# Optimization experiments

Measured on AMD Instinct MI355X. Metric: run time of the kernel, lower is better.

Reference implementation:

```python
import jax, jax.numpy as jnp
import numpy as np

TARGET_RADIUS = 0.99
EPS = 1e-8


def _spectral_norm_wh(W_h):
    # 3-step power iteration (detached, as in torch no_grad), then scale W_h
    # so its spectral radius is ~TARGET_RADIUS. sigma keeps grad through W_h.
    D = W_h.shape[0]
    u = jax.random.normal(jax.random.key(42), (D,), dtype=W_h.dtype)
    u = u / jnp.linalg.norm(u)
    Wd = jax.lax.stop_gradient(W_h)
    v = u
    for _ in range(3):
        v = Wd.T @ u
        v = v / (jnp.linalg.norm(v) + EPS)
        u = Wd @ v
        u = u / (jnp.linalg.norm(u) + EPS)
    sigma = jnp.abs(u @ W_h @ v)
    return W_h * (TARGET_RADIUS / (sigma + EPS))


def setup_inputs() -> dict:
    key = jax.random.key(0)
    T, B, D = 256, 64, 2048
    ks = jax.random.split(key, 5)
    std = 0.02  # ~xavier scale for D=2048 is sqrt(2/(2D))~0.022
    return {
        "x": jax.random.normal(ks[0], (T, B, D), dtype=jnp.float32),
        "z": jax.random.normal(ks[1], (T, B, D), dtype=jnp.float32),
        "h0": jnp.zeros((B, D), dtype=jnp.float32),
        "W_x": jax.random.normal(ks[2], (D, D), dtype=jnp.float32) * std,
        "W_h": jax.random.normal(ks[3], (D, D), dtype=jnp.float32) * std,
        "W_gate": jax.random.normal(ks[4], (D, D), dtype=jnp.float32) * std,
        "b": jnp.zeros((D,), dtype=jnp.float32),
    }


def reference(x, z, h0, W_x, W_h, W_gate, b):
    # h_t = tanh(W_x@x_t + (W_h@h_{t-1}) * sigmoid(W_gate@x_t) + b)
    # out_t = h_t * silu(z_t)
    W_h_eff = _spectral_norm_wh(W_h)
    # Precompute input projections as one big GEMM over T*B (same math).
    xWx = jnp.einsum("tbd,ed->tbe", x, W_x) + b          # [T,B,D]
    gate = jax.nn.sigmoid(jnp.einsum("tbd,ed->tbe", x, W_gate))  # [T,B,D]
    silu_z = jax.nn.silu(z)                               # [T,B,D]

    def step(h_prev, inp):
        xw_t, g_t, sz_t = inp
        Rh = h_prev @ W_h_eff.T                           # [B,D]
        h_new = jnp.tanh(xw_t + Rh * g_t)
        out_t = h_new * sz_t
        return h_new, (h_new, out_t)

    _, (hs, output) = jax.lax.scan(step, h0, (xWx, gate, silu_z))
    h = jnp.concatenate([h0[None], hs], axis=0)           # [T+1,B,D]
    return output, h
```

## Files before the change

### kernel.cpp

```cpp
#include <hip/hip_runtime.h>
#include <hip/hip_cooperative_groups.h>
#include <cstdint>
#include <cmath>

namespace cg = cooperative_groups;


static constexpr int Tt = 256;
static constexpr int Bb = 64;
static constexpr int Dk = 2048;
static constexpr int Mrows = Tt * Bb;
static constexpr float EPSF = 1e-8f;
static constexpr float TARGET_RADIUS = 0.99f;

__device__ __forceinline__ void tf_round(uint32_t& x0, uint32_t& x1, int r) {
    x0 += x1;
    x1 = (x1 << r) | (x1 >> (32 - r));
    x1 ^= x0;
}

__device__ __forceinline__ uint2 threefry2x32(uint32_t ks0, uint32_t ks1,
                                              uint32_t x0, uint32_t x1) {
    uint32_t ks2 = ks0 ^ ks1 ^ 0x1BD11BDAu;
    x0 += ks0; x1 += ks1;
    tf_round(x0,x1,13); tf_round(x0,x1,15); tf_round(x0,x1,26); tf_round(x0,x1,6);
    x0 += ks1; x1 += ks2 + 1u;
    tf_round(x0,x1,17); tf_round(x0,x1,29); tf_round(x0,x1,16); tf_round(x0,x1,24);
    x0 += ks2; x1 += ks0 + 2u;
    tf_round(x0,x1,13); tf_round(x0,x1,15); tf_round(x0,x1,26); tf_round(x0,x1,6);
    x0 += ks0; x1 += ks1 + 3u;
    tf_round(x0,x1,17); tf_round(x0,x1,29); tf_round(x0,x1,16); tf_round(x0,x1,24);
    x0 += ks1; x1 += ks2 + 4u;
    tf_round(x0,x1,13); tf_round(x0,x1,15); tf_round(x0,x1,26); tf_round(x0,x1,6);
    x0 += ks2; x1 += ks0 + 5u;
    return make_uint2(x0, x1);
}

__global__ __launch_bounds__(256) void k_rng(float* __restrict__ u) {
    __shared__ float red[256];
    __shared__ float s_inv;
    float local = 0.f;
    for (int i = threadIdx.x; i < Dk; i += 256) {
        uint2 r = threefry2x32(0u, 42u, 0u, (uint32_t)i);
        uint32_t bits = r.x ^ r.y;
        uint32_t fb = (bits >> 9) | 0x3f800000u;
        float f01 = __uint_as_float(fb) - 1.0f;
        const float lo = -0.99999994f;
        float uu = f01 * (1.0f - lo) + lo;
        uu = fmaxf(lo, uu);
        float g = 1.41421356237f * erfinvf(uu);
        u[i] = g;
        local += g * g;
    }
    red[threadIdx.x] = local;
    __syncthreads();
    for (int s = 128; s > 0; s >>= 1) {
        if (threadIdx.x < s) red[threadIdx.x] += red[threadIdx.x + s];
        __syncthreads();
    }
    if (threadIdx.x == 0) s_inv = 1.0f / sqrtf(red[0]);
    __syncthreads();
    float inv = s_inv;
    for (int i = threadIdx.x; i < Dk; i += 256) u[i] *= inv;
}

__global__ __launch_bounds__(256) void k_matvec_T(const float* __restrict__ W,
                                                  const float* __restrict__ u,
                                                  float* __restrict__ out) {
    __shared__ float us[Dk];
    for (int i = threadIdx.x; i < Dk; i += 256) us[i] = u[i];
    __syncthreads();
    int j = blockIdx.x * 256 + threadIdx.x;
    float acc = 0.f;
    for (int i = 0; i < Dk; ++i) acc += W[(size_t)i * Dk + j] * us[i];
    out[j] = acc;
}

__global__ __launch_bounds__(256) void k_matvec_N(const float* __restrict__ W,
                                                  const float* __restrict__ v,
                                                  float* __restrict__ out) {
    __shared__ float red[256];
    const float* Wr = W + (size_t)blockIdx.x * Dk;
    float acc = 0.f;
    for (int j = threadIdx.x; j < Dk; j += 256) acc += Wr[j] * v[j];
    red[threadIdx.x] = acc;
    __syncthreads();
    for (int s = 128; s > 0; s >>= 1) {
        if (threadIdx.x < s) red[threadIdx.x] += red[threadIdx.x + s];
        __syncthreads();
    }
    if (threadIdx.x == 0) out[blockIdx.x] = red[0];
}

__global__ __launch_bounds__(256) void k_normalize(float* __restrict__ vec) {
    __shared__ float red[256];
    __shared__ float s_inv;
    float acc = 0.f;
    for (int i = threadIdx.x; i < Dk; i += 256) { float x = vec[i]; acc += x * x; }
    red[threadIdx.x] = acc;
    __syncthreads();
    for (int s = 128; s > 0; s >>= 1) {
        if (threadIdx.x < s) red[threadIdx.x] += red[threadIdx.x + s];
        __syncthreads();
    }
    if (threadIdx.x == 0) s_inv = 1.0f / (sqrtf(red[0]) + EPSF);
    __syncthreads();
    float inv = s_inv;
    for (int i = threadIdx.x; i < Dk; i += 256) vec[i] *= inv;
}

__global__ __launch_bounds__(256) void k_sigma(const float* __restrict__ uraw,
                                               float* __restrict__ scale_out) {
    __shared__ float red[256];
    float acc = 0.f;
    for (int i = threadIdx.x; i < Dk; i += 256) { float x = uraw[i]; acc += x * x; }
    red[threadIdx.x] = acc;
    __syncthreads();
    for (int s = 128; s > 0; s >>= 1) {
        if (threadIdx.x < s) red[threadIdx.x] += red[threadIdx.x + s];
        __syncthreads();
    }
    if (threadIdx.x == 0) {
        float ss = red[0];
        float n = sqrtf(ss);
        float sigma = ss / (n + EPSF);
        scale_out[0] = TARGET_RADIUS / (sigma + EPSF);
    }
}

__global__ __launch_bounds__(256, 2) void k_dualgemm(const float* __restrict__ X,
                                                     const float* __restrict__ Wx,
                                                     const float* __restrict__ Wg,
                                                     const float* __restrict__ bias,
                                                     float* __restrict__ xw_out,
                                                     float* __restrict__ gate_out) {
    __shared__ float As [16][132];
    __shared__ float Bxs[16][132];
    __shared__ float Bgs[16][132];

    const int tid = threadIdx.x;
    const int bm = blockIdx.x;
    const int bn = blockIdx.y;
    const int tx = tid & 15;
    const int ty = tid >> 4;

    float accX[8][8] = {};
    float accG[8][8] = {};

    const int lrow = tid >> 2;
    const int lk4  = (tid & 3) << 2;
    const float* Xp0  = X  + (size_t)(bm * 128 + lrow) * Dk + lk4;
    const float* Xp1  = Xp0 + (size_t)64 * Dk;
    const float* Wxp0 = Wx + (size_t)(bn * 128 + lrow) * Dk + lk4;
    const float* Wxp1 = Wxp0 + (size_t)64 * Dk;
    const float* Wgp0 = Wg + (size_t)(bn * 128 + lrow) * Dk + lk4;
    const float* Wgp1 = Wgp0 + (size_t)64 * Dk;

    for (int k0 = 0; k0 < Dk; k0 += 16) {
        float4 xa0 = *(const float4*)(Xp0  + k0);
        float4 xa1 = *(const float4*)(Xp1  + k0);
        float4 wx0 = *(const float4*)(Wxp0 + k0);
        float4 wx1 = *(const float4*)(Wxp1 + k0);
        float4 wg0 = *(const float4*)(Wgp0 + k0);
        float4 wg1 = *(const float4*)(Wgp1 + k0);
        __syncthreads();
        As [lk4 + 0][lrow]      = xa0.x; As [lk4 + 1][lrow]      = xa0.y;
        As [lk4 + 2][lrow]      = xa0.z; As [lk4 + 3][lrow]      = xa0.w;
        As [lk4 + 0][lrow + 64] = xa1.x; As [lk4 + 1][lrow + 64] = xa1.y;
        As [lk4 + 2][lrow + 64] = xa1.z; As [lk4 + 3][lrow + 64] = xa1.w;
        Bxs[lk4 + 0][lrow]      = wx0.x; Bxs[lk4 + 1][lrow]      = wx0.y;
        Bxs[lk4 + 2][lrow]      = wx0.z; Bxs[lk4 + 3][lrow]      = wx0.w;
        Bxs[lk4 + 0][lrow + 64] = wx1.x; Bxs[lk4 + 1][lrow + 64] = wx1.y;
        Bxs[lk4 + 2][lrow + 64] = wx1.z; Bxs[lk4 + 3][lrow + 64] = wx1.w;
        Bgs[lk4 + 0][lrow]      = wg0.x; Bgs[lk4 + 1][lrow]      = wg0.y;
        Bgs[lk4 + 2][lrow]      = wg0.z; Bgs[lk4 + 3][lrow]      = wg0.w;
        Bgs[lk4 + 0][lrow + 64] = wg1.x; Bgs[lk4 + 1][lrow + 64] = wg1.y;
        Bgs[lk4 + 2][lrow + 64] = wg1.z; Bgs[lk4 + 3][lrow + 64] = wg1.w;
        __syncthreads();
#pragma unroll
        for (int kk = 0; kk < 16; ++kk) {
            const float4 a0 = *(const float4*)&As [kk][ty * 8];
            const float4 a1 = *(const float4*)&As [kk][ty * 8 + 4];
            const float4 x0 = *(const float4*)&Bxs[kk][tx * 8];
            const float4 x1 = *(const float4*)&Bxs[kk][tx * 8 + 4];
            const float4 g0 = *(const float4*)&Bgs[kk][tx * 8];
            const float4 g1 = *(const float4*)&Bgs[kk][tx * 8 + 4];
            float av[8] = {a0.x, a0.y, a0.z, a0.w, a1.x, a1.y, a1.z, a1.w};
            float xv[8] = {x0.x, x0.y, x0.z, x0.w, x1.x, x1.y, x1.z, x1.w};
            float gv[8] = {g0.x, g0.y, g0.z, g0.w, g1.x, g1.y, g1.z, g1.w};
#pragma unroll
            for (int i = 0; i < 8; ++i)
#pragma unroll
                for (int j = 0; j < 8; ++j) {
                    accX[i][j] = fmaf(av[i], xv[j], accX[i][j]);
                    accG[i][j] = fmaf(av[i], gv[j], accG[i][j]);
                }
        }
    }

    const int m0 = bm * 128 + ty * 8;
    const int n0 = bn * 128 + tx * 8;
    float4 bv0 = *(const float4*)(bias + n0);
    float4 bv1 = *(const float4*)(bias + n0 + 4);
#pragma unroll
    for (int i = 0; i < 8; ++i) {
        float4 xo0, xo1, go0, go1;
        xo0.x = accX[i][0] + bv0.x; xo0.y = accX[i][1] + bv0.y;
        xo0.z = accX[i][2] + bv0.z; xo0.w = accX[i][3] + bv0.w;
        xo1.x = accX[i][4] + bv1.x; xo1.y = accX[i][5] + bv1.y;
        xo1.z = accX[i][6] + bv1.z; xo1.w = accX[i][7] + bv1.w;
        go0.x = 1.0f / (1.0f + expf(-accG[i][0]));
        go0.y = 1.0f / (1.0f + expf(-accG[i][1]));
        go0.z = 1.0f / (1.0f + expf(-accG[i][2]));
        go0.w = 1.0f / (1.0f + expf(-accG[i][3]));
        go1.x = 1.0f / (1.0f + expf(-accG[i][4]));
        go1.y = 1.0f / (1.0f + expf(-accG[i][5]));
        go1.z = 1.0f / (1.0f + expf(-accG[i][6]));
        go1.w = 1.0f / (1.0f + expf(-accG[i][7]));
        float* xrow = xw_out   + (size_t)(m0 + i) * Dk + n0;
        float* grow = gate_out + (size_t)(m0 + i) * Dk + n0;
        *(float4*)xrow       = xo0;
        *(float4*)(xrow + 4) = xo1;
        *(float4*)grow       = go0;
        *(float4*)(grow + 4) = go1;
    }
}

__global__ __launch_bounds__(256) void k_recur(const float* __restrict__ Wh,
                                               const float* __restrict__ scale_p,
                                               const float* __restrict__ z,
                                               float* __restrict__ out,
                                               float* __restrict__ hbuf) {
    cg::grid_group grid = cg::this_grid();
    __shared__ float Ws[8][2564];

    const int tid = threadIdx.x;
    const int e0 = blockIdx.x * 8;
    const float sc = scale_p[0];

    for (int idx = tid; idx < 8 * 512; idx += 256) {
        const int r = idx >> 9;
        const int c = (idx & 511) << 2;
        float4 w = *(const float4*)(Wh + (size_t)(e0 + r) * Dk + c);
        Ws[r][c + 0] = w.x * sc; Ws[r][c + 1] = w.y * sc;
        Ws[r][c + 2] = w.z * sc; Ws[r][c + 3] = w.w * sc;
    }
    __syncthreads();

    const int e = tid & 7;
    const int brow = tid >> 3;
    const float* wr = &Ws[e][0];
    const size_t BD = (size_t)Bb * Dk;
    const size_t i0 = (size_t)brow * Dk + e0 + e;
    const size_t i1 = i0 + (size_t)32 * Dk;

    for (int t = 0; t < Tt; ++t) {
        const float* hbase = hbuf + (size_t)t * BD;
        float* hg = hbuf + (size_t)(t + 1) * BD;
        float* xo = out  + (size_t)t * BD;
        const float* zt = z + (size_t)t * BD;

        float g0 = hg[i0], g1 = hg[i1];
        float x0 = xo[i0], x1 = xo[i1];
        float z0 = zt[i0], z1 = zt[i1];

        const float* hp0 = hbase + (size_t)brow * Dk;
        const float* hp1 = hp0 + (size_t)32 * Dk;
        float s00 = 0.f, s01 = 0.f, s10 = 0.f, s11 = 0.f;
#pragma unroll 4
        for (int d = 0; d < Dk; d += 8) {
            float4 w0 = *(const float4*)(wr + d);
            float4 w1 = *(const float4*)(wr + d + 4);
            float4 a0 = *(const float4*)(hp0 + d);
            float4 a1 = *(const float4*)(hp0 + d + 4);
            float4 b0 = *(const float4*)(hp1 + d);
            float4 b1 = *(const float4*)(hp1 + d + 4);
            s00 = fmaf(a0.w, w0.w, fmaf(a0.z, w0.z, fmaf(a0.y, w0.y, fmaf(a0.x, w0.x, s00))));
            s01 = fmaf(a1.w, w1.w, fmaf(a1.z, w1.z, fmaf(a1.y, w1.y, fmaf(a1.x, w1.x, s01))));
            s10 = fmaf(b0.w, w0.w, fmaf(b0.z, w0.z, fmaf(b0.y, w0.y, fmaf(b0.x, w0.x, s10))));
            s11 = fmaf(b1.w, w1.w, fmaf(b1.z, w1.z, fmaf(b1.y, w1.y, fmaf(b1.x, w1.x, s11))));
        }
        float r0 = s00 + s01;
        float r1 = s10 + s11;

        float hn0 = tanhf(x0 + r0 * g0);
        float hn1 = tanhf(x1 + r1 * g1);
        float sz0 = z0 / (1.0f + expf(-z0));
        float sz1 = z1 / (1.0f + expf(-z1));
        hg[i0] = hn0; xo[i0] = hn0 * sz0;
        hg[i1] = hn1; xo[i1] = hn1 * sz1;

        if (t + 1 < Tt) grid.sync();
    }
}

extern "C" void kernel_launch(void* const* d_in, const int* in_sizes, int n_in,
                              void* d_out, int out_size, void* d_ws, size_t ws_size,
                              hipStream_t stream) {
    const float* x    = (const float*)d_in[0];
    const float* z    = (const float*)d_in[1];
    const float* h0   = (const float*)d_in[2];
    const float* Wx   = (const float*)d_in[3];
    const float* Wh   = (const float*)d_in[4];
    const float* Wg   = (const float*)d_in[5];
    const float* bias = (const float*)d_in[6];

    float* out  = (float*)d_out;
    float* hbuf = out + (size_t)Tt * Bb * Dk;

    float* ws    = (float*)d_ws;
    float* u     = ws;
    float* v     = ws + 2048;
    float* tmp   = ws + 4096;
    float* scale = ws + 6144;

    const size_t BD = (size_t)Bb * Dk;

    hipMemcpyAsync(hbuf, h0, BD * sizeof(float), hipMemcpyDeviceToDevice, stream);

    k_rng<<<1, 256, 0, stream>>>(u);
    float* uc = u;
    float* ut = tmp;
    for (int it = 0; it < 3; ++it) {
        k_matvec_T<<<8, 256, 0, stream>>>(Wh, uc, v);
        k_normalize<<<1, 256, 0, stream>>>(v);
        k_matvec_N<<<2048, 256, 0, stream>>>(Wh, v, ut);
        if (it < 2) {
            k_normalize<<<1, 256, 0, stream>>>(ut);
            float* t2 = uc; uc = ut; ut = t2;
        }
    }
    k_sigma<<<1, 256, 0, stream>>>(ut, scale);

    dim3 gg(Mrows / 128, Dk / 128);
    k_dualgemm<<<gg, 256, 0, stream>>>(x, Wx, Wg, bias, out, hbuf + BD);

    {
        const float* aWh = Wh;
        const float* aSc = scale;
        const float* aZ  = z;
        float* aOut = out;
        float* aH   = hbuf;
        void* kargs[] = {(void*)&aWh, (void*)&aSc, (void*)&aZ,
                         (void*)&aOut, (void*)&aH};
        hipLaunchCooperativeKernel(k_recur, dim3(256), dim3(256), kargs, 0, stream);
    }
}
```

Before: 20.04 ms.

## Hold W_h slice in registers and split K across threads in recurrence

The cooperative recurrence kernel now runs 512 threads per block. Each thread keeps a 32-wide K-slice of its W_h row in registers, replacing the shared-memory copy of the whole row. Each thread computes partial dot products against all 64 batch rows, and these are reduced with an xor-shuffle butterfly followed by a small shared-memory sum across waves. The aim is to spread the per-step matvec over more threads and remove the long serial 2048-length loop per thread, at the cost of more h loads per thread and extra reduction work. A per-timestep fallback kernel is added in case the cooperative launch fails.

```diff
diff --git a/kernel.cpp b/kernel.cpp
--- a/kernel.cpp
+++ b/kernel.cpp
@@ -226,69 +226,186 @@
     }
 }
 
-__global__ __launch_bounds__(256) void k_recur(const float* __restrict__ Wh,
-                                               const float* __restrict__ scale_p,
-                                               const float* __restrict__ z,
-                                               float* __restrict__ out,
-                                               float* __restrict__ hbuf) {
+__global__ __launch_bounds__(256) void k_step(const float* __restrict__ Wh,
+                                              const float* __restrict__ scale_p,
+                                              const float* __restrict__ z_t,
+                                              float* __restrict__ xw_t,
+                                              const float* __restrict__ h_prev,
+                                              float* __restrict__ hg_t) {
+    __shared__ float Hs[32][36];
+    __shared__ float Ws[32][36];
+    const int tid = threadIdx.x;
+    const int bn = blockIdx.x;
+    const int bb = blockIdx.y;
+    const int tx = tid & 15;
+    const int ty = tid >> 4;
+
+    float a00 = 0.f, a01 = 0.f, a10 = 0.f, a11 = 0.f;
+
+    const int lrow = tid >> 3;
+    const int lk4  = (tid & 7) * 4;
+    const float* Hp = h_prev + (size_t)(bb * 32 + lrow) * Dk + lk4;
+    const float* Wp = Wh     + (size_t)(bn * 32 + lrow) * Dk + lk4;
+
+    for (int k0 = 0; k0 < Dk; k0 += 32) {
+        float4 ha = *(const float4*)(Hp + k0);
+        float4 wa = *(const float4*)(Wp + k0);
+        __syncthreads();
+        Hs[lk4 + 0][lrow] = ha.x; Hs[lk4 + 1][lrow] = ha.y;
+        Hs[lk4 + 2][lrow] = ha.z; Hs[lk4 + 3][lrow] = ha.w;
+        Ws[lk4 + 0][lrow] = wa.x; Ws[lk4 + 1][lrow] = wa.y;
+        Ws[lk4 + 2][lrow] = wa.z; Ws[lk4 + 3][lrow] = wa.w;
+        __syncthreads();
+#pragma unroll
+        for (int kk = 0; kk < 32; ++kk) {
+            float2 hv = *(const float2*)&Hs[kk][ty * 2];
+            float2 wv = *(const float2*)&Ws[kk][tx * 2];
+            a00 += hv.x * wv.x; a01 += hv.x * wv.y;
+            a10 += hv.y * wv.x; a11 += hv.y * wv.y;
+        }
+    }
+
+    const float sc = scale_p[0];
+    const int e0 = bn * 32 + tx * 2;
+    const int b0 = bb * 32 + ty * 2;
+    float acc[2][2] = {{a00, a01}, {a10, a11}};
+#pragma unroll
+    for (int i = 0; i < 2; ++i)
+#pragma unroll
+        for (int j = 0; j < 2; ++j) {
+            size_t idx = (size_t)(b0 + i) * Dk + (e0 + j);
+            float Rh = acc[i][j] * sc;
+            float g = hg_t[idx];
+            float pre = xw_t[idx] + Rh * g;
+            float hn = tanhf(pre);
+            float zv = z_t[idx];
+            float sz = zv / (1.0f + expf(-zv));
+            hg_t[idx] = hn;
+            xw_t[idx] = hn * sz;
+        }
+}
+
+__global__ __launch_bounds__(512, 2) void k_recur(const float* __restrict__ Wh,
+                                                  const float* __restrict__ scale_p,
+                                                  const float* __restrict__ z,
+                                                  float* __restrict__ out,
+                                                  float* __restrict__ hbuf) {
     cg::grid_group grid = cg::this_grid();
-    __shared__ float Ws[8][2564];
+    __shared__ float red[8 * 576];
 
     const int tid = threadIdx.x;
     const int e0 = blockIdx.x * 8;
+    const int c  = tid & 7;
+    const int ks = tid >> 3;
+    const int k0 = ks * 32;
+    const int wv = tid >> 6;
     const float sc = scale_p[0];
 
-    for (int idx = tid; idx < 8 * 512; idx += 256) {
-        const int r = idx >> 9;
-        const int c = (idx & 511) << 2;
-        float4 w = *(const float4*)(Wh + (size_t)(e0 + r) * Dk + c);
-        Ws[r][c + 0] = w.x * sc; Ws[r][c + 1] = w.y * sc;
-        Ws[r][c + 2] = w.z * sc; Ws[r][c + 3] = w.w * sc;
-    }
-    __syncthreads();
-
-    const int e = tid & 7;
-    const int brow = tid >> 3;
-    const float* wr = &Ws[e][0];
+    float w[32];
+    {
+        const float* wp = Wh + (size_t)(e0 + c) * Dk + k0;
+#pragma unroll
+        for (int j = 0; j < 8; ++j) {
+            float4 v = *(const float4*)(wp + 4 * j);
+            w[4*j+0] = v.x * sc; w[4*j+1] = v.y * sc;
+            w[4*j+2] = v.z * sc; w[4*j+3] = v.w * sc;
+        }
+    }
+
+    const int rr = ((tid >> 3) & 1) * 8 + ((tid >> 4) & 1) * 4 + ((tid >> 5) & 1) * 2;
+    const int wbase = wv * 576 + rr * 9 + c;
+
+    const int r_out = tid >> 3;
     const size_t BD = (size_t)Bb * Dk;
-    const size_t i0 = (size_t)brow * Dk + e0 + e;
-    const size_t i1 = i0 + (size_t)32 * Dk;
+    const size_t oidx = (size_t)r_out * Dk + e0 + c;
+    const int rbase = r_out * 9 + c;
+
+    const bool hi3 = (tid & 8)  != 0;
+    const bool hi4 = (tid & 16) != 0;
+    const bool hi5 = (tid & 32) != 0;
 
     for (int t = 0; t < Tt; ++t) {
-        const float* hbase = hbuf + (size_t)t * BD;
+        const float* hb = hbuf + (size_t)t * BD;
         float* hg = hbuf + (size_t)(t + 1) * BD;
         float* xo = out  + (size_t)t * BD;
         const float* zt = z + (size_t)t * BD;
 
-        float g0 = hg[i0], g1 = hg[i1];
-        float x0 = xo[i0], x1 = xo[i1];
-        float z0 = zt[i0], z1 = zt[i1];
-
-        const float* hp0 = hbase + (size_t)brow * Dk;
-        const float* hp1 = hp0 + (size_t)32 * Dk;
-        float s00 = 0.f, s01 = 0.f, s10 = 0.f, s11 = 0.f;
-#pragma unroll 4
-        for (int d = 0; d < Dk; d += 8) {
-            float4 w0 = *(const float4*)(wr + d);
-            float4 w1 = *(const float4*)(wr + d + 4);
-            float4 a0 = *(const float4*)(hp0 + d);
-            float4 a1 = *(const float4*)(hp0 + d + 4);
-            float4 b0 = *(const float4*)(hp1 + d);
-            float4 b1 = *(const float4*)(hp1 + d + 4);
-            s00 = fmaf(a0.w, w0.w, fmaf(a0.z, w0.z, fmaf(a0.y, w0.y, fmaf(a0.x, w0.x, s00))));
-            s01 = fmaf(a1.w, w1.w, fmaf(a1.z, w1.z, fmaf(a1.y, w1.y, fmaf(a1.x, w1.x, s01))));
-            s10 = fmaf(b0.w, w0.w, fmaf(b0.z, w0.z, fmaf(b0.y, w0.y, fmaf(b0.x, w0.x, s10))));
-            s11 = fmaf(b1.w, w1.w, fmaf(b1.z, w1.z, fmaf(b1.y, w1.y, fmaf(b1.x, w1.x, s11))));
-        }
-        float r0 = s00 + s01;
-        float r1 = s10 + s11;
-
-        float hn0 = tanhf(x0 + r0 * g0);
-        float hn1 = tanhf(x1 + r1 * g1);
-        float sz0 = z0 / (1.0f + expf(-z0));
-        float sz1 = z1 / (1.0f + expf(-z1));
-        hg[i0] = hn0; xo[i0] = hn0 * sz0;
-        hg[i1] = hn1; xo[i1] = hn1 * sz1;
+        float gv = hg[oidx];
+        float xv = xo[oidx];
+        float zv = zt[oidx];
+
+#pragma unroll 1
+        for (int g = 0; g < 4; ++g) {
+            float acc[16];
+            const float* hp = hb + (size_t)(g * 16) * Dk + k0;
+#pragma unroll
+            for (int r = 0; r < 16; ++r) {
+                const float* hr = hp + (size_t)r * Dk;
+                float4 h0 = *(const float4*)(hr + 0);
+                float4 h1 = *(const float4*)(hr + 4);
+                float4 h2 = *(const float4*)(hr + 8);
+                float4 h3 = *(const float4*)(hr + 12);
+                float4 h4 = *(const float4*)(hr + 16);
+                float4 h5 = *(const float4*)(hr + 20);
+                float4 h6 = *(const float4*)(hr + 24);
+                float4 h7 = *(const float4*)(hr + 28);
+                float s0 = 0.f, s1 = 0.f;
+                s0 = fmaf(h0.x, w[0], s0);  s1 = fmaf(h0.y, w[1], s1);
+                s0 = fmaf(h0.z, w[2], s0);  s1 = fmaf(h0.w, w[3], s1);
+                s0 = fmaf(h1.x, w[4], s0);  s1 = fmaf(h1.y, w[5], s1);
+                s0 = fmaf(h1.z, w[6], s0);  s1 = fmaf(h1.w, w[7], s1);
+                s0 = fmaf(h2.x, w[8], s0);  s1 = fmaf(h2.y, w[9], s1);
+                s0 = fmaf(h2.z, w[10], s0); s1 = fmaf(h2.w, w[11], s1);
+                s0 = fmaf(h3.x, w[12], s0); s1 = fmaf(h3.y, w[13], s1);
+                s0 = fmaf(h3.z, w[14], s0); s1 = fmaf(h3.w, w[15], s1);
+                s0 = fmaf(h4.x, w[16], s0); s1 = fmaf(h4.y, w[17], s1);
+                s0 = fmaf(h4.z, w[18], s0); s1 = fmaf(h4.w, w[19], s1);
+                s0 = fmaf(h5.x, w[20], s0); s1 = fmaf(h5.y, w[21], s1);
+                s0 = fmaf(h5.z, w[22], s0); s1 = fmaf(h5.w, w[23], s1);
+                s0 = fmaf(h6.x, w[24], s0); s1 = fmaf(h6.y, w[25], s1);
+                s0 = fmaf(h6.z, w[26], s0); s1 = fmaf(h6.w, w[27], s1);
+                s0 = fmaf(h7.x, w[28], s0); s1 = fmaf(h7.y, w[29], s1);
+                s0 = fmaf(h7.z, w[30], s0); s1 = fmaf(h7.w, w[31], s1);
+                acc[r] = s0 + s1;
+            }
+
+            float t8[8];
+#pragma unroll
+            for (int j = 0; j < 8; ++j) {
+                float send = hi3 ? acc[j] : acc[j + 8];
+                float recv = __shfl_xor(send, 8);
+                t8[j] = (hi3 ? acc[j + 8] : acc[j]) + recv;
+            }
+            float t4[4];
+#pragma unroll
+            for (int j = 0; j < 4; ++j) {
+                float send = hi4 ? t8[j] : t8[j + 4];
+                float recv = __shfl_xor(send, 16);
+                t4[j] = (hi4 ? t8[j + 4] : t8[j]) + recv;
+            }
+            float t2[2];
+#pragma unroll
+            for (int j = 0; j < 2; ++j) {
+                float send = hi5 ? t4[j] : t4[j + 2];
+                float recv = __shfl_xor(send, 32);
+                t2[j] = (hi5 ? t4[j + 2] : t4[j]) + recv;
+            }
+
+            red[wbase + g * 144]     = t2[0];
+            red[wbase + g * 144 + 9] = t2[1];
+        }
+        __syncthreads();
+
+        float s = 0.f;
+#pragma unroll
+        for (int v = 0; v < 8; ++v)
+            s += red[v * 576 + rbase];
+
+        float pre = xv + s * gv;
+        float hn = tanhf(pre);
+        float sz = zv / (1.0f + expf(-zv));
+        hg[oidx] = hn;
+        xo[oidx] = hn * sz;
 
         if (t + 1 < Tt) grid.sync();
     }
@@ -335,14 +452,32 @@
     dim3 gg(Mrows / 128, Dk / 128);
     k_dualgemm<<<gg, 256, 0, stream>>>(x, Wx, Wg, bias, out, hbuf + BD);
 
+    bool coop_done = false;
     {
-        const float* aWh = Wh;
-        const float* aSc = scale;
-        const float* aZ  = z;
-        float* aOut = out;
-        float* aH   = hbuf;
-        void* kargs[] = {(void*)&aWh, (void*)&aSc, (void*)&aZ,
-                         (void*)&aOut, (void*)&aH};
-        hipLaunchCooperativeKernel(k_recur, dim3(256), dim3(256), kargs, 0, stream);
-    }
-}
+        int maxActive = 0;
+        hipError_t oe = hipOccupancyMaxActiveBlocksPerMultiprocessor(
+            &maxActive, k_recur, 512, 0);
+        if (oe == hipSuccess && maxActive >= 1) {
+            const float* aWh = Wh;
+            const float* aSc = scale;
+            const float* aZ  = z;
+            float* aOut = out;
+            float* aH   = hbuf;
+            void* kargs[] = {(void*)&aWh, (void*)&aSc, (void*)&aZ,
+                             (void*)&aOut, (void*)&aH};
+            hipError_t le = hipLaunchCooperativeKernel(
+                k_recur, dim3(256), dim3(512), kargs, 0, stream);
+            coop_done = (le == hipSuccess);
+        }
+    }
+    if (!coop_done) {
+        dim3 gs(Dk / 32, Bb / 32);
+        for (int t = 0; t < Tt; ++t) {
+            k_step<<<gs, 256, 0, stream>>>(Wh, scale,
+                                           z + (size_t)t * BD,
+                                           out + (size_t)t * BD,
+                                           hbuf + (size_t)t * BD,
+                                           hbuf + (size_t)(t + 1) * BD);
+        }
+    }
+}
```

Measured after the change: 20.58 ms. 1.03x slower.
